# Performance work log

Measured on AMD Instinct MI355X. Metric: run time of the kernel, lower is better.

Reference implementation:

```python
import jax, jax.numpy as jnp
import numpy as np

EMB_DIM = 384
NUM_HEADS = 12
HEAD_DIM = EMB_DIM // NUM_HEADS
WIN = 7
L = WIN * WIN
B, NW = 64, 64


def get_relative_dis_mat(h, w):
    coord_w, coord_h = np.meshgrid(np.arange(w), np.arange(h))
    index = np.stack([coord_h, coord_w], axis=-1).reshape((-1, 2))
    dis = index[:, None, :] - index[None, :, :]
    dis[:, :, 0] += h - 1
    dis[:, :, 1] += w - 1
    dis = dis[..., 0] * (2 * w - 1) + dis[..., 1]
    return jnp.asarray(dis, dtype=jnp.int32)  # (L, L)


def setup_inputs() -> dict:
    key = jax.random.key(0)
    ks = jax.random.split(key, 6)
    std = 0.02
    x = jax.random.normal(ks[0], (B, NW, L, EMB_DIM), dtype=jnp.float32)
    mask = jnp.zeros((1, NW, 1, L, L), dtype=jnp.float32)
    w_qkv = jax.random.normal(ks[1], (EMB_DIM, 3 * EMB_DIM), dtype=jnp.float32) * std
    b_qkv = jnp.zeros((3 * EMB_DIM,), dtype=jnp.float32)
    w_out = jax.random.normal(ks[2], (EMB_DIM, EMB_DIM), dtype=jnp.float32) * std
    b_out = jnp.zeros((EMB_DIM,), dtype=jnp.float32)
    rel_bias_table = jax.random.normal(ks[3], ((2 * WIN - 1) * (2 * WIN - 1), NUM_HEADS), dtype=jnp.float32) * std
    rel_index = get_relative_dis_mat(WIN, WIN)
    return {"x": x, "mask": mask, "w_qkv": w_qkv, "b_qkv": b_qkv,
            "w_out": w_out, "b_out": b_out, "rel_bias_table": rel_bias_table,
            "rel_index": rel_index}


def reference(x, mask, w_qkv, b_qkv, w_out, b_out, rel_bias_table, rel_index):
    b, nW, l, _ = x.shape
    # QKV projection: (b, nW, L, 3, H, hd)
    qkv = (x @ w_qkv + b_qkv).reshape(b, nW, l, 3, NUM_HEADS, HEAD_DIM)
    q = jnp.transpose(qkv[:, :, :, 0], (0, 1, 3, 2, 4))  # (b, nW, H, L, hd)
    k = jnp.transpose(qkv[:, :, :, 1], (0, 1, 3, 2, 4))
    v = jnp.transpose(qkv[:, :, :, 2], (0, 1, 3, 2, 4))
    scale = 1.0 / jnp.sqrt(jnp.float32(HEAD_DIM))
    score = jnp.einsum('bwhid,bwhjd->bwhij', q, k) * scale  # (b, nW, H, L, L)
    # gathered relative position bias: (L, L, H) -> (H, L, L)
    bias = jnp.transpose(rel_bias_table[rel_index], (2, 0, 1))
    score = score + bias + mask
    alpha = jax.nn.softmax(score, axis=-1)
    context = jnp.einsum('bwhij,bwhjd->bwhid', alpha, v)  # (b, nW, H, L, hd)
    context = jnp.transpose(context, (0, 1, 3, 2, 4)).reshape(b, nW, l, EMB_DIM)
    return context @ w_out + b_out
```

## Files before the change

### kernel.cpp

```cpp
#include <hip/hip_runtime.h>
#include <stdint.h>


#define LTOK 49
#define EMB 384
#define NH 12
#define HD 32
#define SCALE 0.17677669529663687f

typedef short bf16x8 __attribute__((ext_vector_type(8)));
typedef float f32x4 __attribute__((ext_vector_type(4)));

#define XS_OFF   0
#define QO_OFF   49152
#define KO_OFF   57344
#define VO_OFF   65536
#define AL_OFF   73728
#define CTX_OFF  90112
#define BQ_OFF   139264
#define BO_OFF   143872
#define SMEM_TOTAL 145408

#define HSTRIDE 4096

__device__ __forceinline__ unsigned short f2bf(float f) {
    union { float f; unsigned int u; } v; v.f = f;
    return (unsigned short)((v.u + 0x7FFFu + ((v.u >> 16) & 1u)) >> 16);
}

__device__ __forceinline__ int swz768(int r, int g) {
    return r * 768 + (((g & ~7) | ((g ^ r) & 7)) << 4);
}
__device__ __forceinline__ int swz64(int r, int g) {
    return r * 64 + (((g ^ (r >> 1)) & 3) << 4);
}
__device__ __forceinline__ int swz128(int r, int g) {
    return r * 128 + (((g ^ r) & 7) << 4);
}

__global__ __launch_bounds__(256) void setup_k(
    const float* __restrict__ wqkv, const float* __restrict__ wout,
    const float* __restrict__ table, const int* __restrict__ relidx,
    short* __restrict__ wq_frag, short* __restrict__ wo_frag,
    float* __restrict__ bias_m)
{
    int idx = blockIdx.x * 256 + threadIdx.x;
    if (idx < 55296) {
        int ln = idx & 63, t = idx >> 6;
        int nt = t / 12, ks = t % 12;
        int c  = nt * 16 + (ln & 15);
        int k0 = ks * 32 + (ln >> 4) * 8;
        short4 p0, p1;
        p0.x = (short)f2bf(wqkv[(k0 + 0) * 1152 + c]);
        p0.y = (short)f2bf(wqkv[(k0 + 1) * 1152 + c]);
        p0.z = (short)f2bf(wqkv[(k0 + 2) * 1152 + c]);
        p0.w = (short)f2bf(wqkv[(k0 + 3) * 1152 + c]);
        p1.x = (short)f2bf(wqkv[(k0 + 4) * 1152 + c]);
        p1.y = (short)f2bf(wqkv[(k0 + 5) * 1152 + c]);
        p1.z = (short)f2bf(wqkv[(k0 + 6) * 1152 + c]);
        p1.w = (short)f2bf(wqkv[(k0 + 7) * 1152 + c]);
        *(short4*)(wq_frag + idx * 8)     = p0;
        *(short4*)(wq_frag + idx * 8 + 4) = p1;
    } else if (idx < 73728) {
        int i2 = idx - 55296;
        int ln = i2 & 63, t = i2 >> 6;
        int nt = t / 12, ks = t % 12;
        int c  = nt * 16 + (ln & 15);
        int k0 = ks * 32 + (ln >> 4) * 8;
        short4 p0, p1;
        p0.x = (short)f2bf(wout[(k0 + 0) * 384 + c]);
        p0.y = (short)f2bf(wout[(k0 + 1) * 384 + c]);
        p0.z = (short)f2bf(wout[(k0 + 2) * 384 + c]);
        p0.w = (short)f2bf(wout[(k0 + 3) * 384 + c]);
        p1.x = (short)f2bf(wout[(k0 + 4) * 384 + c]);
        p1.y = (short)f2bf(wout[(k0 + 5) * 384 + c]);
        p1.z = (short)f2bf(wout[(k0 + 6) * 384 + c]);
        p1.w = (short)f2bf(wout[(k0 + 7) * 384 + c]);
        *(short4*)(wo_frag + i2 * 8)     = p0;
        *(short4*)(wo_frag + i2 * 8 + 4) = p1;
    } else if (idx < 102540) {
        int t = idx - 73728;
        int h = t / 2401, ij = t % 2401;
        bias_m[h * 2401 + ij] = table[relidx[ij] * 12 + h];
    }
}

__global__ __launch_bounds__(512) void wmha_fused(
    const float* __restrict__ x, const float* __restrict__ mask,
    const float* __restrict__ b_qkv, const float* __restrict__ b_out,
    const short* __restrict__ wq_frag, const short* __restrict__ wo_frag,
    const float* __restrict__ bias_m, float* __restrict__ out)
{
    extern __shared__ __align__(16) char smem[];
    const int tid  = threadIdx.x;
    const int lane = tid & 63;
    const int wv   = tid >> 6;
    const int l15  = lane & 15;
    const int lg   = lane >> 4;
    const int win  = blockIdx.x;
    const int wi   = win & 63;
    const f32x4 z4 = {0.f, 0.f, 0.f, 0.f};

    {
        const float* xw = x + (size_t)win * (LTOK * EMB);
        #pragma unroll 1
        for (int i = tid; i < (64 * EMB) / 4; i += 512) {
            int e = i << 2;
            int r = e / EMB, c = e % EMB;
            float4 v = make_float4(0.f, 0.f, 0.f, 0.f);
            if (r < LTOK) v = *(const float4*)(xw + e);
            short4 p;
            p.x = (short)f2bf(v.x); p.y = (short)f2bf(v.y);
            p.z = (short)f2bf(v.z); p.w = (short)f2bf(v.w);
            *(short4*)(smem + XS_OFF + swz768(r, c >> 3) + (c & 7) * 2) = p;
        }
        for (int i = tid; i < 3 * EMB; i += 512)
            ((float*)(smem + BQ_OFF))[i] = b_qkv[i];
        if (tid < EMB)
            ((float*)(smem + BO_OFF))[tid] = b_out[tid];
    }
    __syncthreads();

    const int mtq  = wv & 3;
    const int ntg  = wv >> 2;
    const int arow = mtq * 16 + l15;

    for (int grp = 0; grp < 6; ++grp) {
        const int h0 = grp * 2;

        f32x4 acc[6];
        int boff[6], wch[6], whh[6], wdd[6];
        #pragma unroll
        for (int u = 0; u < 6; ++u) {
            acc[u] = z4;
            int lnt = ntg * 6 + u;
            int which = lnt >> 2, hh = (lnt >> 1) & 1, t = lnt & 1;
            int gnt = which * 24 + (h0 + hh) * 2 + t;
            boff[u] = gnt * 6144 + lane * 8;
            wch[u] = which; whh[u] = hh; wdd[u] = t * 16 + l15;
        }
        bf16x8 a_cur = *(const bf16x8*)(smem + XS_OFF + swz768(arow, lg));
        bf16x8 b_cur[6];
        #pragma unroll
        for (int u = 0; u < 6; ++u)
            b_cur[u] = *(const bf16x8*)(wq_frag + boff[u]);
        #pragma unroll 2
        for (int ks = 0; ks < 11; ++ks) {
            bf16x8 a_nx = *(const bf16x8*)(smem + XS_OFF + swz768(arow, (ks + 1) * 4 + lg));
            bf16x8 b_nx[6];
            #pragma unroll
            for (int u = 0; u < 6; ++u)
                b_nx[u] = *(const bf16x8*)(wq_frag + boff[u] + (ks + 1) * 512);
            #pragma unroll
            for (int u = 0; u < 6; ++u)
                acc[u] = __builtin_amdgcn_mfma_f32_16x16x32_bf16(a_cur, b_cur[u], acc[u], 0, 0, 0);
            a_cur = a_nx;
            #pragma unroll
            for (int u = 0; u < 6; ++u) b_cur[u] = b_nx[u];
        }
        #pragma unroll
        for (int u = 0; u < 6; ++u)
            acc[u] = __builtin_amdgcn_mfma_f32_16x16x32_bf16(a_cur, b_cur[u], acc[u], 0, 0, 0);

        {
            const float* BQ = (const float*)(smem + BQ_OFF);
            const int tk0 = mtq * 16 + lg * 4;
            #pragma unroll
            for (int u = 0; u < 6; ++u) {
                int d = wdd[u];
                float bias = BQ[wch[u] * EMB + (h0 + whh[u]) * HD + d];
                if (wch[u] == 0) {
                    #pragma unroll
                    for (int q = 0; q < 4; ++q)
                        *(unsigned short*)(smem + QO_OFF + whh[u] * HSTRIDE +
                                           swz64(tk0 + q, d >> 3) + (d & 7) * 2)
                            = f2bf((acc[u][q] + bias) * SCALE);
                } else if (wch[u] == 1) {
                    #pragma unroll
                    for (int q = 0; q < 4; ++q)
                        *(unsigned short*)(smem + KO_OFF + whh[u] * HSTRIDE +
                                           swz64(tk0 + q, d >> 3) + (d & 7) * 2)
                            = f2bf(acc[u][q] + bias);
                } else {
                    float v0 = (tk0 + 0 < LTOK) ? acc[u][0] + bias : 0.f;
                    float v1 = (tk0 + 1 < LTOK) ? acc[u][1] + bias : 0.f;
                    float v2 = (tk0 + 2 < LTOK) ? acc[u][2] + bias : 0.f;
                    float v3 = (tk0 + 3 < LTOK) ? acc[u][3] + bias : 0.f;
                    short4 p;
                    p.x = (short)f2bf(v0); p.y = (short)f2bf(v1);
                    p.z = (short)f2bf(v2); p.w = (short)f2bf(v3);
                    *(short4*)(smem + VO_OFF + whh[u] * HSTRIDE +
                               swz128(d, tk0 >> 3) + (tk0 & 7) * 2) = p;
                }
            }
        }
        __syncthreads();

        {
            const int hh  = wv >> 2;
            const int amt = wv & 3;
            const int h   = h0 + hh;
            bf16x8 aq = *(const bf16x8*)(smem + QO_OFF + hh * HSTRIDE +
                                         swz64(amt * 16 + l15, lg));
            f32x4 s[4];
            #pragma unroll
            for (int nt = 0; nt < 4; ++nt) {
                bf16x8 bk = *(const bf16x8*)(smem + KO_OFF + hh * HSTRIDE +
                                             swz64(nt * 16 + l15, lg));
                s[nt] = __builtin_amdgcn_mfma_f32_16x16x32_bf16(aq, bk, z4, 0, 0, 0);
            }
            const int rl0 = lg * 4;
            #pragma unroll
            for (int nt = 0; nt < 4; ++nt) {
                int j = nt * 16 + l15;
                #pragma unroll
                for (int q = 0; q < 4; ++q) {
                    int i = amt * 16 + rl0 + q;
                    float sv = s[nt][q];
                    if (j < LTOK) {
                        if (i < LTOK) {
                            int ij = i * 49 + j;
                            sv += bias_m[h * 2401 + ij] + mask[wi * 2401 + ij];
                        }
                    } else sv = -1e30f;
                    s[nt][q] = sv;
                }
            }
            float m4[4];
            #pragma unroll
            for (int q = 0; q < 4; ++q)
                m4[q] = fmaxf(fmaxf(s[0][q], s[1][q]), fmaxf(s[2][q], s[3][q]));
            #pragma unroll
            for (int off = 1; off <= 8; off <<= 1) {
                #pragma unroll
                for (int q = 0; q < 4; ++q)
                    m4[q] = fmaxf(m4[q], __shfl_xor(m4[q], off));
            }
            float sum4[4] = {0.f, 0.f, 0.f, 0.f};
            #pragma unroll
            for (int nt = 0; nt < 4; ++nt) {
                #pragma unroll
                for (int q = 0; q < 4; ++q) {
                    float e = __expf(s[nt][q] - m4[q]);
                    s[nt][q] = e;
                    sum4[q] += e;
                }
            }
            #pragma unroll
            for (int off = 1; off <= 8; off <<= 1) {
                #pragma unroll
                for (int q = 0; q < 4; ++q)
                    sum4[q] += __shfl_xor(sum4[q], off);
            }
            float inv4[4];
            #pragma unroll
            for (int q = 0; q < 4; ++q) inv4[q] = 1.f / sum4[q];

            #pragma unroll
            for (int nt = 0; nt < 4; ++nt) {
                int j = nt * 16 + l15;
                #pragma unroll
                for (int q = 0; q < 4; ++q)
                    *(unsigned short*)(smem + AL_OFF + wv * 2048 +
                                       swz128(rl0 + q, j >> 3) + (j & 7) * 2)
                        = f2bf(s[nt][q]);
            }
            #pragma unroll
            for (int dt = 0; dt < 2; ++dt) {
                f32x4 c = z4;
                #pragma unroll
                for (int k2 = 0; k2 < 2; ++k2) {
                    bf16x8 aa = *(const bf16x8*)(smem + AL_OFF + wv * 2048 +
                                                 swz128(l15, lg + k2 * 4));
                    bf16x8 bv = *(const bf16x8*)(smem + VO_OFF + hh * HSTRIDE +
                                                 swz128(dt * 16 + l15, lg + k2 * 4));
                    c = __builtin_amdgcn_mfma_f32_16x16x32_bf16(aa, bv, c, 0, 0, 0);
                }
                int ec = h * HD + dt * 16 + l15;
                #pragma unroll
                for (int q = 0; q < 4; ++q) {
                    int tok = amt * 16 + rl0 + q;
                    *(unsigned short*)(smem + CTX_OFF + swz768(tok, ec >> 3) + (ec & 7) * 2)
                        = f2bf(c[q] * inv4[q]);
                }
            }
        }
        __syncthreads();
    }

    {
        const float* BO = (const float*)(smem + BO_OFF);
        const int tk0 = mtq * 16 + lg * 4;
        #pragma unroll 1
        for (int pass = 0; pass < 2; ++pass) {
            const int nt0 = ntg * 12 + pass * 6;
            f32x4 acc[6];
            #pragma unroll
            for (int u = 0; u < 6; ++u) acc[u] = z4;
            bf16x8 a_cur = *(const bf16x8*)(smem + CTX_OFF + swz768(arow, lg));
            bf16x8 b_cur[6];
            #pragma unroll
            for (int u = 0; u < 6; ++u)
                b_cur[u] = *(const bf16x8*)(wo_frag + ((nt0 + u) * 768 + lane) * 8);
            #pragma unroll 2
            for (int ks = 0; ks < 11; ++ks) {
                bf16x8 a_nx = *(const bf16x8*)(smem + CTX_OFF + swz768(arow, (ks + 1) * 4 + lg));
                bf16x8 b_nx[6];
                #pragma unroll
                for (int u = 0; u < 6; ++u)
                    b_nx[u] = *(const bf16x8*)(wo_frag + ((nt0 + u) * 768 + lane) * 8 + (ks + 1) * 512);
                #pragma unroll
                for (int u = 0; u < 6; ++u)
                    acc[u] = __builtin_amdgcn_mfma_f32_16x16x32_bf16(a_cur, b_cur[u], acc[u], 0, 0, 0);
                a_cur = a_nx;
                #pragma unroll
                for (int u = 0; u < 6; ++u) b_cur[u] = b_nx[u];
            }
            #pragma unroll
            for (int u = 0; u < 6; ++u)
                acc[u] = __builtin_amdgcn_mfma_f32_16x16x32_bf16(a_cur, b_cur[u], acc[u], 0, 0, 0);
            #pragma unroll
            for (int u = 0; u < 6; ++u) {
                int col = (nt0 + u) * 16 + l15;
                float bo = BO[col];
                #pragma unroll
                for (int q = 0; q < 4; ++q) {
                    int tok = tk0 + q;
                    if (tok < LTOK)
                        out[((size_t)win * LTOK + tok) * EMB + col] = acc[u][q] + bo;
                }
            }
        }
    }
}

extern "C" void kernel_launch(void* const* d_in, const int* in_sizes, int n_in,
                              void* d_out, int out_size, void* d_ws, size_t ws_size,
                              hipStream_t stream)
{
    const float* x      = (const float*)d_in[0];
    const float* mask   = (const float*)d_in[1];
    const float* w_qkv  = (const float*)d_in[2];
    const float* b_qkv  = (const float*)d_in[3];
    const float* w_out  = (const float*)d_in[4];
    const float* b_out  = (const float*)d_in[5];
    const float* table  = (const float*)d_in[6];
    const int*   relidx = (const int*)d_in[7];
    float* out = (float*)d_out;

    short* wq_frag = (short*)d_ws;
    short* wo_frag = wq_frag + 442368;
    float* bias_m  = (float*)((char*)d_ws + 1179648);
    size_t need = 1179648 + 115248;
    if (ws_size < need) return;

    setup_k<<<401, 256, 0, stream>>>(w_qkv, w_out, table, relidx,
                                     wq_frag, wo_frag, bias_m);

    hipFuncSetAttribute(reinterpret_cast<const void*>(wmha_fused),
                        hipFuncAttributeMaxDynamicSharedMemorySize, SMEM_TOTAL);
    wmha_fused<<<4096, 512, SMEM_TOTAL, stream>>>(x, mask, b_qkv, b_out,
                                                  wq_frag, wo_frag, bias_m, out);
}
```

Baseline: 1.726 ms.

## Pre-convert x to bf16 MFMA fragments and shrink LDS for higher occupancy

Adds a separate kernel that converts each window of x to bf16 laid out in MFMA A-fragment order in workspace. The main kernel then reads A operands straight from global memory instead of staging x in LDS. Q/K tiles are also packed more tightly, cutting LDS from about 145KB to 81KB so more blocks can be resident per CU. The cost is an extra pass that writes and rereads a 200MB bf16 copy of x. The new path depends on the workspace being large enough, and falls back to the old kernel otherwise.

```diff
diff --git a/kernel.cpp b/kernel.cpp
--- a/kernel.cpp
+++ b/kernel.cpp
@@ -11,18 +11,6 @@
 typedef short bf16x8 __attribute__((ext_vector_type(8)));
 typedef float f32x4 __attribute__((ext_vector_type(4)));
 
-#define XS_OFF   0
-#define QO_OFF   49152
-#define KO_OFF   57344
-#define VO_OFF   65536
-#define AL_OFF   73728
-#define CTX_OFF  90112
-#define BQ_OFF   139264
-#define BO_OFF   143872
-#define SMEM_TOTAL 145408
-
-#define HSTRIDE 4096
-
 __device__ __forceinline__ unsigned short f2bf(float f) {
     union { float f; unsigned int u; } v; v.f = f;
     return (unsigned short)((v.u + 0x7FFFu + ((v.u >> 16) & 1u)) >> 16);
@@ -37,6 +25,17 @@
 __device__ __forceinline__ int swz128(int r, int g) {
     return r * 128 + (((g ^ r) & 7) << 4);
 }
+
+#define W_QO   0
+#define W_KO   6272
+#define W_VO   12544
+#define W_CTX  20736
+#define W_AL   58368
+#define W_BQ   74752
+#define W_BO   79360
+#define W_SMEM 80896
+#define QSTR   3136
+#define VSTR   4096
 
 __global__ __launch_bounds__(256) void setup_k(
     const float* __restrict__ wqkv, const float* __restrict__ wout,
@@ -85,6 +84,282 @@
     }
 }
 
+__global__ __launch_bounds__(256) void setup_x(
+    const float* __restrict__ x, short* __restrict__ x_frag)
+{
+    int win = blockIdx.x;
+    const float* xw = x + (size_t)win * (LTOK * EMB);
+    short* xo = x_frag + (size_t)win * 24576;
+    #pragma unroll 1
+    for (int t = 0; t < 12; ++t) {
+        int v = t * 256 + threadIdx.x;
+        int lane = v & 63, ks = (v >> 6) % 12, mtq = v / 768;
+        int row = mtq * 16 + (lane & 15);
+        int k0 = ks * 32 + (lane >> 4) * 8;
+        short4 p0 = {0, 0, 0, 0}, p1 = {0, 0, 0, 0};
+        if (row < LTOK) {
+            float4 a = *(const float4*)(xw + row * EMB + k0);
+            float4 b = *(const float4*)(xw + row * EMB + k0 + 4);
+            p0.x = (short)f2bf(a.x); p0.y = (short)f2bf(a.y);
+            p0.z = (short)f2bf(a.z); p0.w = (short)f2bf(a.w);
+            p1.x = (short)f2bf(b.x); p1.y = (short)f2bf(b.y);
+            p1.z = (short)f2bf(b.z); p1.w = (short)f2bf(b.w);
+        }
+        *(short4*)(xo + v * 8)     = p0;
+        *(short4*)(xo + v * 8 + 4) = p1;
+    }
+}
+
+__global__ __launch_bounds__(512, 4) void wmha_v2(
+    const short* __restrict__ x_frag, const float* __restrict__ mask,
+    const float* __restrict__ b_qkv, const float* __restrict__ b_out,
+    const short* __restrict__ wq_frag, const short* __restrict__ wo_frag,
+    const float* __restrict__ bias_m, float* __restrict__ out)
+{
+    extern __shared__ __align__(16) char smem[];
+    const int tid  = threadIdx.x;
+    const int lane = tid & 63;
+    const int wv   = tid >> 6;
+    const int l15  = lane & 15;
+    const int lg   = lane >> 4;
+    const int win  = blockIdx.x;
+    const int wi   = win & 63;
+    const f32x4 z4 = {0.f, 0.f, 0.f, 0.f};
+
+    for (int i = tid; i < 3 * EMB; i += 512)
+        ((float*)(smem + W_BQ))[i] = b_qkv[i];
+    if (tid < EMB)
+        ((float*)(smem + W_BO))[tid] = b_out[tid];
+    __syncthreads();
+
+    const int mtq  = wv & 3;
+    const int ntg  = wv >> 2;
+    const int arow = mtq * 16 + l15;
+    const short* xf = x_frag + (size_t)win * 24576 + mtq * 6144 + lane * 8;
+
+    for (int grp = 0; grp < 6; ++grp) {
+        const int h0 = grp * 2;
+
+        f32x4 acc[6];
+        int boff[6], wch[6], whh[6], wdd[6];
+        #pragma unroll
+        for (int u = 0; u < 6; ++u) {
+            acc[u] = z4;
+            int lnt = ntg * 6 + u;
+            int which = lnt >> 2, hh = (lnt >> 1) & 1, t = lnt & 1;
+            int gnt = which * 24 + (h0 + hh) * 2 + t;
+            boff[u] = gnt * 6144 + lane * 8;
+            wch[u] = which; whh[u] = hh; wdd[u] = t * 16 + l15;
+        }
+        bf16x8 a_cur = *(const bf16x8*)(xf);
+        bf16x8 b_cur[6];
+        #pragma unroll
+        for (int u = 0; u < 6; ++u)
+            b_cur[u] = *(const bf16x8*)(wq_frag + boff[u]);
+        #pragma unroll 2
+        for (int ks = 0; ks < 11; ++ks) {
+            bf16x8 a_nx = *(const bf16x8*)(xf + (ks + 1) * 512);
+            bf16x8 b_nx[6];
+            #pragma unroll
+            for (int u = 0; u < 6; ++u)
+                b_nx[u] = *(const bf16x8*)(wq_frag + boff[u] + (ks + 1) * 512);
+            #pragma unroll
+            for (int u = 0; u < 6; ++u)
+                acc[u] = __builtin_amdgcn_mfma_f32_16x16x32_bf16(a_cur, b_cur[u], acc[u], 0, 0, 0);
+            a_cur = a_nx;
+            #pragma unroll
+            for (int u = 0; u < 6; ++u) b_cur[u] = b_nx[u];
+        }
+        #pragma unroll
+        for (int u = 0; u < 6; ++u)
+            acc[u] = __builtin_amdgcn_mfma_f32_16x16x32_bf16(a_cur, b_cur[u], acc[u], 0, 0, 0);
+
+        {
+            const float* BQ = (const float*)(smem + W_BQ);
+            const int tk0 = mtq * 16 + lg * 4;
+            #pragma unroll
+            for (int u = 0; u < 6; ++u) {
+                int d = wdd[u];
+                float bias = BQ[wch[u] * EMB + (h0 + whh[u]) * HD + d];
+                if (wch[u] == 0) {
+                    #pragma unroll
+                    for (int q = 0; q < 4; ++q)
+                        if (tk0 + q < LTOK)
+                            *(unsigned short*)(smem + W_QO + whh[u] * QSTR +
+                                               swz64(tk0 + q, d >> 3) + (d & 7) * 2)
+                                = f2bf((acc[u][q] + bias) * SCALE);
+                } else if (wch[u] == 1) {
+                    #pragma unroll
+                    for (int q = 0; q < 4; ++q)
+                        if (tk0 + q < LTOK)
+                            *(unsigned short*)(smem + W_KO + whh[u] * QSTR +
+                                               swz64(tk0 + q, d >> 3) + (d & 7) * 2)
+                                = f2bf(acc[u][q] + bias);
+                } else {
+                    float v0 = (tk0 + 0 < LTOK) ? acc[u][0] + bias : 0.f;
+                    float v1 = (tk0 + 1 < LTOK) ? acc[u][1] + bias : 0.f;
+                    float v2 = (tk0 + 2 < LTOK) ? acc[u][2] + bias : 0.f;
+                    float v3 = (tk0 + 3 < LTOK) ? acc[u][3] + bias : 0.f;
+                    short4 p;
+                    p.x = (short)f2bf(v0); p.y = (short)f2bf(v1);
+                    p.z = (short)f2bf(v2); p.w = (short)f2bf(v3);
+                    *(short4*)(smem + W_VO + whh[u] * VSTR +
+                               swz128(d, tk0 >> 3) + (tk0 & 7) * 2) = p;
+                }
+            }
+        }
+        __syncthreads();
+
+        {
+            const int hh  = wv >> 2;
+            const int amt = wv & 3;
+            const int h   = h0 + hh;
+            bf16x8 aq = *(const bf16x8*)(smem + W_QO + hh * QSTR +
+                                         swz64(amt * 16 + l15, lg));
+            f32x4 s[4];
+            #pragma unroll
+            for (int nt = 0; nt < 4; ++nt) {
+                bf16x8 bk = *(const bf16x8*)(smem + W_KO + hh * QSTR +
+                                             swz64(nt * 16 + l15, lg));
+                s[nt] = __builtin_amdgcn_mfma_f32_16x16x32_bf16(aq, bk, z4, 0, 0, 0);
+            }
+            const int rl0 = lg * 4;
+            #pragma unroll
+            for (int nt = 0; nt < 4; ++nt) {
+                int j = nt * 16 + l15;
+                #pragma unroll
+                for (int q = 0; q < 4; ++q) {
+                    int i = amt * 16 + rl0 + q;
+                    float sv = s[nt][q];
+                    if (j < LTOK) {
+                        if (i < LTOK) {
+                            int ij = i * 49 + j;
+                            sv += bias_m[h * 2401 + ij] + mask[wi * 2401 + ij];
+                        }
+                    } else sv = -1e30f;
+                    s[nt][q] = sv;
+                }
+            }
+            float m4[4];
+            #pragma unroll
+            for (int q = 0; q < 4; ++q)
+                m4[q] = fmaxf(fmaxf(s[0][q], s[1][q]), fmaxf(s[2][q], s[3][q]));
+            #pragma unroll
+            for (int off = 1; off <= 8; off <<= 1) {
+                #pragma unroll
+                for (int q = 0; q < 4; ++q)
+                    m4[q] = fmaxf(m4[q], __shfl_xor(m4[q], off));
+            }
+            float sum4[4] = {0.f, 0.f, 0.f, 0.f};
+            #pragma unroll
+            for (int nt = 0; nt < 4; ++nt) {
+                #pragma unroll
+                for (int q = 0; q < 4; ++q) {
+                    float e = __expf(s[nt][q] - m4[q]);
+                    s[nt][q] = e;
+                    sum4[q] += e;
+                }
+            }
+            #pragma unroll
+            for (int off = 1; off <= 8; off <<= 1) {
+                #pragma unroll
+                for (int q = 0; q < 4; ++q)
+                    sum4[q] += __shfl_xor(sum4[q], off);
+            }
+            float inv4[4];
+            #pragma unroll
+            for (int q = 0; q < 4; ++q) inv4[q] = 1.f / sum4[q];
+
+            #pragma unroll
+            for (int nt = 0; nt < 4; ++nt) {
+                int j = nt * 16 + l15;
+                #pragma unroll
+                for (int q = 0; q < 4; ++q)
+                    *(unsigned short*)(smem + W_AL + wv * 2048 +
+                                       swz128(rl0 + q, j >> 3) + (j & 7) * 2)
+                        = f2bf(s[nt][q]);
+            }
+            #pragma unroll
+            for (int dt = 0; dt < 2; ++dt) {
+                f32x4 c = z4;
+                #pragma unroll
+                for (int k2 = 0; k2 < 2; ++k2) {
+                    bf16x8 aa = *(const bf16x8*)(smem + W_AL + wv * 2048 +
+                                                 swz128(l15, lg + k2 * 4));
+                    bf16x8 bv = *(const bf16x8*)(smem + W_VO + hh * VSTR +
+                                                 swz128(dt * 16 + l15, lg + k2 * 4));
+                    c = __builtin_amdgcn_mfma_f32_16x16x32_bf16(aa, bv, c, 0, 0, 0);
+                }
+                int ec = h * HD + dt * 16 + l15;
+                #pragma unroll
+                for (int q = 0; q < 4; ++q) {
+                    int tok = amt * 16 + rl0 + q;
+                    if (tok < LTOK)
+                        *(unsigned short*)(smem + W_CTX + swz768(tok, ec >> 3) + (ec & 7) * 2)
+                            = f2bf(c[q] * inv4[q]);
+                }
+            }
+        }
+        __syncthreads();
+    }
+
+    {
+        const float* BO = (const float*)(smem + W_BO);
+        const int tk0 = mtq * 16 + lg * 4;
+        #pragma unroll 1
+        for (int pass = 0; pass < 2; ++pass) {
+            const int nt0 = ntg * 12 + pass * 6;
+            f32x4 acc[6];
+            #pragma unroll
+            for (int u = 0; u < 6; ++u) acc[u] = z4;
+            bf16x8 a_cur = *(const bf16x8*)(smem + W_CTX + swz768(arow, lg));
+            bf16x8 b_cur[6];
+            #pragma unroll
+            for (int u = 0; u < 6; ++u)
+                b_cur[u] = *(const bf16x8*)(wo_frag + ((nt0 + u) * 768 + lane) * 8);
+            #pragma unroll 2
+            for (int ks = 0; ks < 11; ++ks) {
+                bf16x8 a_nx = *(const bf16x8*)(smem + W_CTX + swz768(arow, (ks + 1) * 4 + lg));
+                bf16x8 b_nx[6];
+                #pragma unroll
+                for (int u = 0; u < 6; ++u)
+                    b_nx[u] = *(const bf16x8*)(wo_frag + ((nt0 + u) * 768 + lane) * 8 + (ks + 1) * 512);
+                #pragma unroll
+                for (int u = 0; u < 6; ++u)
+                    acc[u] = __builtin_amdgcn_mfma_f32_16x16x32_bf16(a_cur, b_cur[u], acc[u], 0, 0, 0);
+                a_cur = a_nx;
+                #pragma unroll
+                for (int u = 0; u < 6; ++u) b_cur[u] = b_nx[u];
+            }
+            #pragma unroll
+            for (int u = 0; u < 6; ++u)
+                acc[u] = __builtin_amdgcn_mfma_f32_16x16x32_bf16(a_cur, b_cur[u], acc[u], 0, 0, 0);
+            #pragma unroll
+            for (int u = 0; u < 6; ++u) {
+                int col = (nt0 + u) * 16 + l15;
+                float bo = BO[col];
+                #pragma unroll
+                for (int q = 0; q < 4; ++q) {
+                    int tok = tk0 + q;
+                    if (tok < LTOK)
+                        out[((size_t)win * LTOK + tok) * EMB + col] = acc[u][q] + bo;
+                }
+            }
+        }
+    }
+}
+
+#define XS_OFF   0
+#define QO_OFF   49152
+#define KO_OFF   57344
+#define VO_OFF   65536
+#define AL_OFF   73728
+#define CTX_OFF  90112
+#define BQ_OFF   139264
+#define BO_OFF   143872
+#define SMEM_TOTAL 145408
+#define HSTRIDE 4096
+
 __global__ __launch_bounds__(512) void wmha_fused(
     const float* __restrict__ x, const float* __restrict__ mask,
     const float* __restrict__ b_qkv, const float* __restrict__ b_out,
@@ -127,7 +402,6 @@
 
     for (int grp = 0; grp < 6; ++grp) {
         const int h0 = grp * 2;
-
         f32x4 acc[6];
         int boff[6], wch[6], whh[6], wdd[6];
         #pragma unroll
@@ -351,14 +625,24 @@
     short* wq_frag = (short*)d_ws;
     short* wo_frag = wq_frag + 442368;
     float* bias_m  = (float*)((char*)d_ws + 1179648);
-    size_t need = 1179648 + 115248;
-    if (ws_size < need) return;
+    short* x_frag  = (short*)((char*)d_ws + 1294896);
+    size_t need_small = 1294896;
+    size_t need_big   = 1294896 + (size_t)4096 * 24576 * 2;
+    if (ws_size < need_small) return;
 
     setup_k<<<401, 256, 0, stream>>>(w_qkv, w_out, table, relidx,
                                      wq_frag, wo_frag, bias_m);
 
-    hipFuncSetAttribute(reinterpret_cast<const void*>(wmha_fused),
-                        hipFuncAttributeMaxDynamicSharedMemorySize, SMEM_TOTAL);
-    wmha_fused<<<4096, 512, SMEM_TOTAL, stream>>>(x, mask, b_qkv, b_out,
-                                                  wq_frag, wo_frag, bias_m, out);
-}
+    if (ws_size >= need_big) {
+        setup_x<<<4096, 256, 0, stream>>>(x, x_frag);
+        hipFuncSetAttribute(reinterpret_cast<const void*>(wmha_v2),
+                            hipFuncAttributeMaxDynamicSharedMemorySize, W_SMEM);
+        wmha_v2<<<4096, 512, W_SMEM, stream>>>(x_frag, mask, b_qkv, b_out,
+                                               wq_frag, wo_frag, bias_m, out);
+    } else {
+        hipFuncSetAttribute(reinterpret_cast<const void*>(wmha_fused),
+                            hipFuncAttributeMaxDynamicSharedMemorySize, SMEM_TOTAL);
+        wmha_fused<<<4096, 512, SMEM_TOTAL, stream>>>(x, mask, b_qkv, b_out,
+                                                      wq_frag, wo_frag, bias_m, out);
+    }
+}
```

After: 2.911 ms. +68.6%, slower.
